# Kernel optimization log

Measured on AMD Instinct MI355X. Metric: run time of the kernel, lower is better.

The kernel has to match this reference:

```python
import jax, jax.numpy as jnp
import numpy as np

N_NODES = 50000
N_EDGES = 800000
DIMS = [64, 128, 128, 64]  # input_dim -> hidden_dims
OUT_DIM = 64
N_CLASSES = 10


def _linear_params(key, in_f, out_f):
    kw, kb = jax.random.split(key)
    bound = 1.0 / np.sqrt(in_f)
    W = jax.random.uniform(kw, (out_f, in_f), jnp.float32, -bound, bound)
    b = jax.random.uniform(kb, (out_f,), jnp.float32, -bound, bound)
    return W, b


def setup_inputs() -> dict:
    key = jax.random.key(0)
    ks = jax.random.split(key, 8)
    x = jax.random.normal(ks[0], (N_NODES, DIMS[0]), jnp.float32)
    edge_index = jax.random.randint(ks[1], (2, N_EDGES), 0, N_NODES, jnp.int32)
    W1, b1 = _linear_params(ks[2], DIMS[0], DIMS[1])
    W2, b2 = _linear_params(ks[3], DIMS[1], DIMS[2])
    W3, b3 = _linear_params(ks[4], DIMS[2], DIMS[3])
    Wp, bp = _linear_params(ks[5], DIMS[3], OUT_DIM)
    Wc, bc = _linear_params(ks[6], DIMS[3], N_CLASSES)
    return {"node_features": x, "edge_index": edge_index,
            "W1": W1, "b1": b1, "W2": W2, "b2": b2, "W3": W3, "b3": b3,
            "Wp": Wp, "bp": bp, "Wc": Wc, "bc": bc}


def _conv_layer(x, src, dst, W, b):
    # mean-aggregate neighbor features via segment_sum over destination nodes
    n = x.shape[0]
    agg = jax.ops.segment_sum(x[src], dst, num_segments=n)  # [N, F]
    deg = jax.ops.segment_sum(jnp.ones_like(dst, jnp.float32), dst, num_segments=n)
    deg = jnp.maximum(deg, 1.0)
    agg = agg / deg[:, None]
    return jax.nn.relu((agg + x) @ W.T + b)


def reference(node_features, edge_index, W1, b1, W2, b2, W3, b3, Wp, bp, Wc, bc):
    src, dst = edge_index[0], edge_index[1]
    x = node_features
    # dropout is identity in eval mode
    x = _conv_layer(x, src, dst, W1, b1)
    x = _conv_layer(x, src, dst, W2, b2)
    x = _conv_layer(x, src, dst, W3, b3)
    node_embeddings = x
    next_event = x @ Wp.T + bp
    event_classes = x @ Wc.T + bc
    return node_embeddings, next_event, event_classes
```

## Files before the change

### kernel.cpp

```cpp
#include <hip/hip_runtime.h>
#include <hip/hip_bf16.h>

typedef __attribute__((ext_vector_type(8))) short short8;
typedef __attribute__((ext_vector_type(4))) float floatx4;

#define NB   196
#define NBLK 256

__device__ __forceinline__ float bf_lo(unsigned int u) { return __uint_as_float(u << 16); }
__device__ __forceinline__ float bf_hi(unsigned int u) { return __uint_as_float(u & 0xffff0000u); }

__device__ __forceinline__ unsigned short f2bf_rne(float f) {
    unsigned u = __float_as_uint(f);
    unsigned rb = (u >> 16) & 1u;
    u += 0x7fffu + rb;
    return (unsigned short)(u >> 16);
}
__device__ __forceinline__ unsigned int pack_bf2(float x, float y) {
    return (unsigned int)f2bf_rne(x) | ((unsigned int)f2bf_rne(y) << 16);
}

__device__ __forceinline__ void acc4(unsigned long long v, float& f0, float& f1, float& f2, float& f3) {
    unsigned ua = (unsigned)v, ub = (unsigned)(v >> 32);
    f0 += bf_lo(ua); f1 += bf_hi(ua); f2 += bf_lo(ub); f3 += bf_hi(ub);
}


__global__ __launch_bounds__(256) void prep_kernel(const int* __restrict__ dst,
                                                   int* __restrict__ blockcnt,
                                                   int E,
                                                   const float* __restrict__ x,
                                                   const float* __restrict__ W1,
                                                   const float* __restrict__ W2,
                                                   const float* __restrict__ W3,
                                                   const float* __restrict__ Wp, const float* __restrict__ bp,
                                                   const float* __restrict__ Wc, const float* __restrict__ bc,
                                                   unsigned int* __restrict__ xb,
                                                   unsigned int* __restrict__ W1b,
                                                   unsigned int* __restrict__ W2b,
                                                   unsigned int* __restrict__ W3b,
                                                   unsigned int* __restrict__ Whb,
                                                   float* __restrict__ hbias,
                                                   int nx) {
    if ((int)blockIdx.x < NBLK) {
        __shared__ int hist[NB];
        for (int i = threadIdx.x; i < NB; i += 256) hist[i] = 0;
        __syncthreads();
        const int chunk = (E + NBLK - 1) / NBLK;
        const int lo = blockIdx.x * chunk;
        const int hi = min(lo + chunk, E);
        for (int e = lo + threadIdx.x; e < hi; e += 256)
            atomicAdd(&hist[dst[e] >> 8], 1);
        __syncthreads();
        for (int i = threadIdx.x; i < NB; i += 256)
            blockcnt[i * NBLK + blockIdx.x] = hist[i];
        return;
    }
    int i = (blockIdx.x - NBLK) * 256 + threadIdx.x;
    const int T0 = nx;
    const int T1 = T0 + 4096;
    const int T2 = T1 + 8192;
    const int T3 = T2 + 4096;
    const int T4 = T3 + 2560;
    const int T5 = T4 + 80;
    if (i < T0) {
        float2 f = ((const float2*)x)[i];
        xb[i] = pack_bf2(f.x, f.y);
    } else if (i < T1) {
        float2 f = ((const float2*)W1)[i - T0];
        W1b[i - T0] = pack_bf2(f.x, f.y);
    } else if (i < T2) {
        float2 f = ((const float2*)W2)[i - T1];
        W2b[i - T1] = pack_bf2(f.x, f.y);
    } else if (i < T3) {
        float2 f = ((const float2*)W3)[i - T2];
        W3b[i - T2] = pack_bf2(f.x, f.y);
    } else if (i < T4) {
        int j = i - T3;
        int r = j >> 5, c = (j & 31) * 2;
        float v0 = 0.f, v1 = 0.f;
        if (r < 64)      { v0 = Wp[r * 64 + c]; v1 = Wp[r * 64 + c + 1]; }
        else if (r < 74) { v0 = Wc[(r - 64) * 64 + c]; v1 = Wc[(r - 64) * 64 + c + 1]; }
        Whb[j] = pack_bf2(v0, v1);
    } else if (i < T5) {
        int j = i - T4;
        float v = 0.f;
        if (j < 64)      v = bp[j];
        else if (j < 74) v = bc[j - 64];
        hbias[j] = v;
    }
}


__global__ __launch_bounds__(256) void partial_sum_kernel(const int* __restrict__ v,
                                                          int* __restrict__ partial, int n) {
    __shared__ int s[256];
    int t = threadIdx.x;
    int i = blockIdx.x * 256 + t;
    s[t] = (i < n) ? v[i] : 0;
    __syncthreads();
    for (int off = 128; off > 0; off >>= 1) {
        if (t < off) s[t] += s[t + off];
        __syncthreads();
    }
    if (t == 0) partial[blockIdx.x] = s[0];
}

__global__ __launch_bounds__(256) void local_scan_kernel(const int* __restrict__ v,
                                                         const int* __restrict__ partial,
                                                         int* __restrict__ base,
                                                         int nblocks, int n) {
    __shared__ int sp[256];
    __shared__ int s[256];
    int t = threadIdx.x;
    sp[t] = (t < nblocks) ? partial[t] : 0;
    __syncthreads();
    for (int off = 1; off < 256; off <<= 1) {
        int u = (t >= off) ? sp[t - off] : 0;
        __syncthreads();
        sp[t] += u;
        __syncthreads();
    }
    const int blockbase = (blockIdx.x == 0) ? 0 : sp[blockIdx.x - 1];
    if (blockIdx.x == 0 && t == 0) base[n] = sp[nblocks - 1];

    int i = blockIdx.x * 256 + t;
    int w = (i < n) ? v[i] : 0;
    s[t] = w;
    __syncthreads();
    for (int off = 1; off < 256; off <<= 1) {
        int u = (t >= off) ? s[t - off] : 0;
        __syncthreads();
        s[t] += u;
        __syncthreads();
    }
    if (i < n) base[i] = blockbase + s[t] - w;
}


__global__ __launch_bounds__(256) void binC_kernel(const int* __restrict__ src,
                                                   const int* __restrict__ dst,
                                                   const int* __restrict__ base,
                                                   unsigned int* __restrict__ pairs, int E) {
    __shared__ int bbase[NB];
    __shared__ int cur[NB];
    for (int i = threadIdx.x; i < NB; i += 256) {
        bbase[i] = base[i * NBLK + blockIdx.x];
        cur[i] = 0;
    }
    __syncthreads();
    const int chunk = (E + NBLK - 1) / NBLK;
    const int lo = blockIdx.x * chunk;
    const int hi = min(lo + chunk, E);
    for (int e = lo + threadIdx.x; e < hi; e += 256) {
        int d = dst[e];
        int b = d >> 8;
        int r = atomicAdd(&cur[b], 1);
        pairs[bbase[b] + r] = ((unsigned)d << 16) | (unsigned)src[e];
    }
}


__global__ __launch_bounds__(256) void bucketD_kernel(const unsigned int* __restrict__ pairs,
                                                      const int* __restrict__ base,
                                                      int* __restrict__ offsets,
                                                      unsigned short* __restrict__ csr_src,
                                                      int E, int n) {
    __shared__ int cnt[256];
    __shared__ int loc[256];
    const int b = blockIdx.x;
    const int start = base[b * NBLK];
    const int end   = base[(b + 1) * NBLK];
    const int t = threadIdx.x;

    cnt[t] = 0;
    __syncthreads();
    for (int i = start + t; i < end; i += 256)
        atomicAdd(&cnt[(pairs[i] >> 16) & 255], 1);
    __syncthreads();

    loc[t] = cnt[t];
    __syncthreads();
    for (int off = 1; off < 256; off <<= 1) {
        int u = (t >= off) ? loc[t - off] : 0;
        __syncthreads();
        loc[t] += u;
        __syncthreads();
    }
    const int excl = (t == 0) ? 0 : loc[t - 1];

    const int d = (b << 8) + t;
    if (d < n) offsets[d] = start + excl;
    if (b == 0 && t == 0) offsets[n] = E;

    __syncthreads();
    cnt[t] = excl;
    __syncthreads();
    for (int i = start + t; i < end; i += 256) {
        unsigned pr = pairs[i];
        int j = (pr >> 16) & 255;
        int p = atomicAdd(&cnt[j], 1);
        csr_src[start + p] = (unsigned short)(pr & 0xffffu);
    }
}


template <int F_IN, int F_OUT, int MODE>
__global__ __launch_bounds__(512) void fused_agg_gemm_kernel(
        const unsigned long long* __restrict__ xt,
        const int* __restrict__ offsets,
        const unsigned short* __restrict__ csr_src,
        const unsigned short* __restrict__ Wb,
        const float* __restrict__ bias,
        unsigned short* __restrict__ Yb,
        float* __restrict__ Yf,
        float* __restrict__ nev, float* __restrict__ cls,
        const unsigned short* __restrict__ Whb, const float* __restrict__ hbias,
        int n) {
    constexpr int KC   = F_IN / 32;
    constexpr int XSTR = F_IN / 4;
    constexpr int HSTR = F_IN + 8;
    __shared__ __align__(16) unsigned short Ht[32 * HSTR];
    __shared__ __align__(16) unsigned short Yt[(MODE == 3) ? 32 * 72 : 16];

    const int lane = threadIdx.x & 63;
    const int wv   = threadIdx.x >> 6;
    const int m0   = blockIdx.x * 32;

    if (F_IN == 64) {
        const int g   = lane >> 4;
        const int c   = lane & 15;
        const int row = wv * 4 + g;
        const int node = m0 + row;
        int ns = 0, ne = 0;
        if (node < n) { ns = offsets[node]; ne = offsets[node + 1]; }
        const int cnt = ne - ns;
        unsigned long long sv = (node < n) ? xt[(size_t)node * XSTR + c] : 0ull;

        int mc = cnt;
        mc = max(mc, __shfl(mc, lane ^ 16, 64));
        mc = max(mc, __shfl(mc, lane ^ 32, 64));

        float s0 = 0.f, s1 = 0.f, s2 = 0.f, s3 = 0.f;
        int ii0 = ns + c;
        if (cnt > 0) { if (ii0 >= ne) ii0 = ne - 1; } else ii0 = 0;
        int idx = (mc > 0) ? (int)csr_src[ii0] : 0;

        for (int base = 0; base < mc; base += 16) {
            int idxN = 0;
            if (base + 16 < mc) {
                int ii = ns + base + 16 + c;
                if (cnt > 0) { if (ii >= ne) ii = ne - 1; } else ii = 0;
                idxN = csr_src[ii];
            }
            unsigned long long v[16];
#pragma unroll
            for (int q = 0; q < 16; ++q) {
                int nb = __shfl(idx, g * 16 + q, 64);
                if (base + q < cnt) v[q] = xt[(size_t)nb * XSTR + c];
            }
#pragma unroll
            for (int q = 0; q < 16; ++q)
                if (base + q < cnt) acc4(v[q], s0, s1, s2, s3);
            idx = idxN;
        }
        float inv = 1.0f / fmaxf((float)cnt, 1.0f);
        unsigned ua = (unsigned)sv, ub = (unsigned)(sv >> 32);
        unsigned o0 = pack_bf2(s0 * inv + bf_lo(ua), s1 * inv + bf_hi(ua));
        unsigned o1 = pack_bf2(s2 * inv + bf_lo(ub), s3 * inv + bf_hi(ub));
        *(unsigned long long*)&Ht[row * HSTR + c * 4] =
            ((unsigned long long)o1 << 32) | o0;
    } else {
        const int g = lane >> 5;
        const int c = lane & 31;
        const int row0 = wv * 4 + g;
        const int row1 = wv * 4 + 2 + g;
        const int node0 = m0 + row0, node1 = m0 + row1;
        int ns0 = 0, ne0 = 0, ns1 = 0, ne1 = 0;
        if (node0 < n) { ns0 = offsets[node0]; ne0 = offsets[node0 + 1]; }
        if (node1 < n) { ns1 = offsets[node1]; ne1 = offsets[node1 + 1]; }
        const int cnt0 = ne0 - ns0, cnt1 = ne1 - ns1;
        unsigned long long sv0 = (node0 < n) ? xt[(size_t)node0 * XSTR + c] : 0ull;
        unsigned long long sv1 = (node1 < n) ? xt[(size_t)node1 * XSTR + c] : 0ull;
        int mc0 = max(cnt0, __shfl(cnt0, lane ^ 32, 64));
        int mc1 = max(cnt1, __shfl(cnt1, lane ^ 32, 64));
        int iiA = ns0 + (c & 15);
        if (cnt0 > 0) { if (iiA >= ne0) iiA = ne0 - 1; } else iiA = 0;
        int iiB = ns1 + (c & 15);
        if (cnt1 > 0) { if (iiB >= ne1) iiB = ne1 - 1; } else iiB = 0;
        int idx0 = (mc0 > 0) ? (int)csr_src[iiA] : 0;
        int idx1 = (mc1 > 0) ? (int)csr_src[iiB] : 0;

        {
            float s0 = 0.f, s1 = 0.f, s2 = 0.f, s3 = 0.f;
            int idx = idx0;
            for (int base = 0; base < mc0; base += 16) {
                int idxN = 0;
                if (base + 16 < mc0) {
                    int ii = ns0 + base + 16 + (c & 15);
                    if (cnt0 > 0) { if (ii >= ne0) ii = ne0 - 1; } else ii = 0;
                    idxN = csr_src[ii];
                }
                unsigned long long v[16];
#pragma unroll
                for (int q = 0; q < 16; ++q) {
                    int nb = __shfl(idx, g * 32 + q, 64);
                    if (base + q < cnt0) v[q] = xt[(size_t)nb * XSTR + c];
                }
#pragma unroll
                for (int q = 0; q < 16; ++q)
                    if (base + q < cnt0) acc4(v[q], s0, s1, s2, s3);
                idx = idxN;
            }
            float inv = 1.0f / fmaxf((float)cnt0, 1.0f);
            unsigned ua = (unsigned)sv0, ub = (unsigned)(sv0 >> 32);
            unsigned o0 = pack_bf2(s0 * inv + bf_lo(ua), s1 * inv + bf_hi(ua));
            unsigned o1 = pack_bf2(s2 * inv + bf_lo(ub), s3 * inv + bf_hi(ub));
            *(unsigned long long*)&Ht[row0 * HSTR + c * 4] =
                ((unsigned long long)o1 << 32) | o0;
        }
        {
            float s0 = 0.f, s1 = 0.f, s2 = 0.f, s3 = 0.f;
            int idx = idx1;
            for (int base = 0; base < mc1; base += 16) {
                int idxN = 0;
                if (base + 16 < mc1) {
                    int ii = ns1 + base + 16 + (c & 15);
                    if (cnt1 > 0) { if (ii >= ne1) ii = ne1 - 1; } else ii = 0;
                    idxN = csr_src[ii];
                }
                unsigned long long v[16];
#pragma unroll
                for (int q = 0; q < 16; ++q) {
                    int nb = __shfl(idx, g * 32 + q, 64);
                    if (base + q < cnt1) v[q] = xt[(size_t)nb * XSTR + c];
                }
#pragma unroll
                for (int q = 0; q < 16; ++q)
                    if (base + q < cnt1) acc4(v[q], s0, s1, s2, s3);
                idx = idxN;
            }
            float inv = 1.0f / fmaxf((float)cnt1, 1.0f);
            unsigned ua = (unsigned)sv1, ub = (unsigned)(sv1 >> 32);
            unsigned o0 = pack_bf2(s0 * inv + bf_lo(ua), s1 * inv + bf_hi(ua));
            unsigned o1 = pack_bf2(s2 * inv + bf_lo(ub), s3 * inv + bf_hi(ub));
            *(unsigned long long*)&Ht[row1 * HSTR + c * 4] =
                ((unsigned long long)o1 << 32) | o0;
        }
    }
    __syncthreads();

    const int quad = lane >> 4;
    const int r16  = lane & 15;

    if (MODE == 0) {
        const int rowg = wv & 1;
        const int cg0  = (wv >> 1) * 2;
        short8 a[KC];
#pragma unroll
        for (int c = 0; c < KC; ++c)
            a[c] = *(const short8*)&Ht[(16 * rowg + r16) * HSTR + 32 * c + quad * 8];

        floatx4 acc[2];
#pragma unroll
        for (int j = 0; j < 2; ++j)
#pragma unroll
            for (int r = 0; r < 4; ++r) acc[j][r] = 0.f;

#pragma unroll
        for (int j = 0; j < 2; ++j)
#pragma unroll
            for (int c = 0; c < KC; ++c) {
                short8 b = *(const short8*)&Wb[(size_t)(16 * (cg0 + j) + r16) * F_IN + 32 * c + quad * 8];
                acc[j] = __builtin_amdgcn_mfma_f32_16x16x32_bf16(a[c], b, acc[j], 0, 0, 0);
            }

#pragma unroll
        for (int r = 0; r < 4; ++r) {
            const int mm = m0 + 16 * rowg + quad * 4 + r;
            if (mm >= n) continue;
#pragma unroll
            for (int j = 0; j < 2; ++j) {
                const int o = 16 * (cg0 + j) + r16;
                Yb[(size_t)mm * F_OUT + o] = f2bf_rne(fmaxf(acc[j][r] + bias[o], 0.f));
            }
        }
    } else {
        const int rowg = wv & 1;
        const int cg   = wv >> 1;
        short8 a[KC];
#pragma unroll
        for (int c = 0; c < KC; ++c)
            a[c] = *(const short8*)&Ht[(16 * rowg + r16) * HSTR + 32 * c + quad * 8];

        floatx4 acc;
#pragma unroll
        for (int r = 0; r < 4; ++r) acc[r] = 0.f;

#pragma unroll
        for (int c = 0; c < KC; ++c) {
            short8 b = *(const short8*)&Wb[(size_t)(16 * cg + r16) * F_IN + 32 * c + quad * 8];
            acc = __builtin_amdgcn_mfma_f32_16x16x32_bf16(a[c], b, acc, 0, 0, 0);
        }

#pragma unroll
        for (int r = 0; r < 4; ++r) {
            const int lr = 16 * rowg + quad * 4 + r;
            const int mm = m0 + lr;
            const int o  = 16 * cg + r16;
            if (mm < n) {
                float v = fmaxf(acc[r] + bias[o], 0.f);
                Yf[(size_t)mm * 64 + o] = v;
                Yt[lr * 72 + o] = f2bf_rne(v);
            } else {
                Yt[lr * 72 + o] = 0;
            }
        }
        __syncthreads();

        for (int t = wv; t < 10; t += 8) {
            const int rg  = t & 1;
            const int cg2 = t >> 1;
            short8 a2[2];
#pragma unroll
            for (int c = 0; c < 2; ++c)
                a2[c] = *(const short8*)&Yt[(16 * rg + r16) * 72 + 32 * c + quad * 8];

            floatx4 acc2;
#pragma unroll
            for (int r = 0; r < 4; ++r) acc2[r] = 0.f;

#pragma unroll
            for (int c = 0; c < 2; ++c) {
                short8 b = *(const short8*)&Whb[(size_t)(16 * cg2 + r16) * 64 + 32 * c + quad * 8];
                acc2 = __builtin_amdgcn_mfma_f32_16x16x32_bf16(a2[c], b, acc2, 0, 0, 0);
            }

#pragma unroll
            for (int r = 0; r < 4; ++r) {
                const int mm = m0 + 16 * rg + quad * 4 + r;
                if (mm >= n) continue;
                const int o = 16 * cg2 + r16;
                float v = acc2[r] + hbias[o];
                if (o < 64)      nev[(size_t)mm * 64 + o] = v;
                else if (o < 74) cls[(size_t)mm * 10 + (o - 64)] = v;
            }
        }
    }
}


extern "C" void kernel_launch(void* const* d_in, const int* in_sizes, int n_in,
                              void* d_out, int out_size, void* d_ws, size_t ws_size,
                              hipStream_t stream) {
    const float* x  = (const float*)d_in[0];
    const int*   ei = (const int*)d_in[1];
    const float* W1 = (const float*)d_in[2];
    const float* b1 = (const float*)d_in[3];
    const float* W2 = (const float*)d_in[4];
    const float* b2 = (const float*)d_in[5];
    const float* W3 = (const float*)d_in[6];
    const float* b3 = (const float*)d_in[7];
    const float* Wp = (const float*)d_in[8];
    const float* bp = (const float*)d_in[9];
    const float* Wc = (const float*)d_in[10];
    const float* bc = (const float*)d_in[11];

    const int n = in_sizes[0] / 64;
    const int E = in_sizes[1] / 2;
    const int* src = ei;
    const int* dst = ei + E;

    const int items = NB * NBLK;
    const int nScan = (items + 255) / 256;

    int* blockcnt = (int*)d_ws;
    int* base     = blockcnt + items;
    int* partial  = base + items + 1;
    int* offsets  = partial + 256;
    unsigned int*   pairs   = (unsigned int*)(offsets + n + 1);
    unsigned short* csr_src = (unsigned short*)(pairs + E);
    uintptr_t p = (uintptr_t)(csr_src + E);
    p = (p + 255) & ~(uintptr_t)255;
    unsigned int* Hb  = (unsigned int*)p;
    unsigned int* Yb  = Hb + (size_t)n * 64;
    unsigned int* xb  = Yb + (size_t)n * 64;
    unsigned int* W1b = xb + (size_t)n * 32;
    unsigned int* W2b = W1b + 4096;
    unsigned int* W3b = W2b + 8192;
    unsigned int* Whb = W3b + 4096;
    float* hbias = (float*)(Whb + 2560);

    float* out_emb = (float*)d_out;
    float* out_nev = out_emb + (size_t)n * 64;
    float* out_cls = out_nev + (size_t)n * 64;

    const int convTotal = n * 32 + 4096 + 8192 + 4096 + 2560 + 80;
    const int convBlocks = (convTotal + 255) / 256;
    prep_kernel<<<NBLK + convBlocks, 256, 0, stream>>>(
        dst, blockcnt, E,
        x, W1, W2, W3, Wp, bp, Wc, bc, xb, W1b, W2b, W3b, Whb, hbias, n * 32);

    partial_sum_kernel<<<nScan, 256, 0, stream>>>(blockcnt, partial, items);
    local_scan_kernel<<<nScan, 256, 0, stream>>>(blockcnt, partial, base, nScan, items);

    binC_kernel<<<NBLK, 256, 0, stream>>>(src, dst, base, pairs, E);
    bucketD_kernel<<<NB, 256, 0, stream>>>(pairs, base, offsets, csr_src, E, n);

    const int gF = (n + 31) / 32;

    fused_agg_gemm_kernel<64, 128, 0><<<gF, 512, 0, stream>>>(
        (const unsigned long long*)xb, offsets, csr_src,
        (const unsigned short*)W1b, b1, (unsigned short*)Hb,
        nullptr, nullptr, nullptr, nullptr, nullptr, n);

    fused_agg_gemm_kernel<128, 128, 0><<<gF, 512, 0, stream>>>(
        (const unsigned long long*)Hb, offsets, csr_src,
        (const unsigned short*)W2b, b2, (unsigned short*)Yb,
        nullptr, nullptr, nullptr, nullptr, nullptr, n);

    fused_agg_gemm_kernel<128, 64, 3><<<gF, 512, 0, stream>>>(
        (const unsigned long long*)Yb, offsets, csr_src,
        (const unsigned short*)W3b, b3, nullptr,
        out_emb, out_nev, out_cls, (const unsigned short*)Whb, hbias, n);
}
```

Measured before the change: 230.2 us.

## Split fused aggregate+GEMM into column-sliced gather kernels and separate MFMA GEMMs

Replaces each fused aggregate-then-GEMM kernel with two kernels. The first aggregates neighbours per node over a column slice of 8 uint64 lanes, spreading the edges across 8 lane groups and combining them with a shuffle reduction. The second runs a standalone MFMA GEMM that reads the aggregated bf16 rows from a workspace buffer. Slicing columns is meant to keep each slice's gather working set in cache and balance work across skewed degrees. The cost is three extra launches and an extra write and read of the aggregated matrix through global memory.

```diff
diff --git a/kernel.cpp b/kernel.cpp
--- a/kernel.cpp
+++ b/kernel.cpp
@@ -205,243 +205,164 @@
 }
 
 
-template <int F_IN, int F_OUT, int MODE>
-__global__ __launch_bounds__(512) void fused_agg_gemm_kernel(
+template <int F_IN, int NSLICE>
+__global__ __launch_bounds__(256) void agg_slice_kernel(
         const unsigned long long* __restrict__ xt,
         const int* __restrict__ offsets,
         const unsigned short* __restrict__ csr_src,
-        const unsigned short* __restrict__ Wb,
-        const float* __restrict__ bias,
-        unsigned short* __restrict__ Yb,
-        float* __restrict__ Yf,
-        float* __restrict__ nev, float* __restrict__ cls,
-        const unsigned short* __restrict__ Whb, const float* __restrict__ hbias,
+        unsigned long long* __restrict__ hb,
         int n) {
-    constexpr int KC   = F_IN / 32;
     constexpr int XSTR = F_IN / 4;
-    constexpr int HSTR = F_IN + 8;
-    __shared__ __align__(16) unsigned short Ht[32 * HSTR];
-    __shared__ __align__(16) unsigned short Yt[(MODE == 3) ? 32 * 72 : 16];
-
     const int lane = threadIdx.x & 63;
     const int wv   = threadIdx.x >> 6;
-    const int m0   = blockIdx.x * 32;
-
-    if (F_IN == 64) {
-        const int g   = lane >> 4;
-        const int c   = lane & 15;
-        const int row = wv * 4 + g;
-        const int node = m0 + row;
-        int ns = 0, ne = 0;
-        if (node < n) { ns = offsets[node]; ne = offsets[node + 1]; }
+    const int s    = blockIdx.x % NSLICE;
+    const int nb   = blockIdx.x / NSLICE;
+    const int g    = lane >> 3;
+    const int c    = lane & 7;
+    const int col  = s * 8 + c;
+
+#pragma unroll 1
+    for (int i = 0; i < 4; ++i) {
+        const int node = nb * 16 + wv * 4 + i;
+        if (node >= n) continue;
+        const int ns = offsets[node];
+        const int ne = offsets[node + 1];
         const int cnt = ne - ns;
-        unsigned long long sv = (node < n) ? xt[(size_t)node * XSTR + c] : 0ull;
-
-        int mc = cnt;
-        mc = max(mc, __shfl(mc, lane ^ 16, 64));
-        mc = max(mc, __shfl(mc, lane ^ 32, 64));
+        unsigned long long sv = xt[(size_t)node * XSTR + col];
 
         float s0 = 0.f, s1 = 0.f, s2 = 0.f, s3 = 0.f;
-        int ii0 = ns + c;
-        if (cnt > 0) { if (ii0 >= ne) ii0 = ne - 1; } else ii0 = 0;
-        int idx = (mc > 0) ? (int)csr_src[ii0] : 0;
-
-        for (int base = 0; base < mc; base += 16) {
-            int idxN = 0;
-            if (base + 16 < mc) {
-                int ii = ns + base + 16 + c;
-                if (cnt > 0) { if (ii >= ne) ii = ne - 1; } else ii = 0;
-                idxN = csr_src[ii];
+        for (int base = 0; base < cnt; base += 64) {
+            int ii = ns + base + lane; if (ii >= ne) ii = ne - 1;
+            int idx = csr_src[ii];
+            int m = cnt - base; if (m > 64) m = 64;
+            unsigned long long v[8];
+#pragma unroll
+            for (int q = 0; q < 8; ++q) {
+                int nb2 = __shfl(idx, q * 8 + g, 64);
+                if (q * 8 + g < m) v[q] = xt[(size_t)nb2 * XSTR + col];
             }
-            unsigned long long v[16];
-#pragma unroll
-            for (int q = 0; q < 16; ++q) {
-                int nb = __shfl(idx, g * 16 + q, 64);
-                if (base + q < cnt) v[q] = xt[(size_t)nb * XSTR + c];
-            }
-#pragma unroll
-            for (int q = 0; q < 16; ++q)
-                if (base + q < cnt) acc4(v[q], s0, s1, s2, s3);
-            idx = idxN;
+#pragma unroll
+            for (int q = 0; q < 8; ++q)
+                if (q * 8 + g < m) acc4(v[q], s0, s1, s2, s3);
         }
-        float inv = 1.0f / fmaxf((float)cnt, 1.0f);
-        unsigned ua = (unsigned)sv, ub = (unsigned)(sv >> 32);
-        unsigned o0 = pack_bf2(s0 * inv + bf_lo(ua), s1 * inv + bf_hi(ua));
-        unsigned o1 = pack_bf2(s2 * inv + bf_lo(ub), s3 * inv + bf_hi(ub));
-        *(unsigned long long*)&Ht[row * HSTR + c * 4] =
-            ((unsigned long long)o1 << 32) | o0;
-    } else {
-        const int g = lane >> 5;
-        const int c = lane & 31;
-        const int row0 = wv * 4 + g;
-        const int row1 = wv * 4 + 2 + g;
-        const int node0 = m0 + row0, node1 = m0 + row1;
-        int ns0 = 0, ne0 = 0, ns1 = 0, ne1 = 0;
-        if (node0 < n) { ns0 = offsets[node0]; ne0 = offsets[node0 + 1]; }
-        if (node1 < n) { ns1 = offsets[node1]; ne1 = offsets[node1 + 1]; }
-        const int cnt0 = ne0 - ns0, cnt1 = ne1 - ns1;
-        unsigned long long sv0 = (node0 < n) ? xt[(size_t)node0 * XSTR + c] : 0ull;
-        unsigned long long sv1 = (node1 < n) ? xt[(size_t)node1 * XSTR + c] : 0ull;
-        int mc0 = max(cnt0, __shfl(cnt0, lane ^ 32, 64));
-        int mc1 = max(cnt1, __shfl(cnt1, lane ^ 32, 64));
-        int iiA = ns0 + (c & 15);
-        if (cnt0 > 0) { if (iiA >= ne0) iiA = ne0 - 1; } else iiA = 0;
-        int iiB = ns1 + (c & 15);
-        if (cnt1 > 0) { if (iiB >= ne1) iiB = ne1 - 1; } else iiB = 0;
-        int idx0 = (mc0 > 0) ? (int)csr_src[iiA] : 0;
-        int idx1 = (mc1 > 0) ? (int)csr_src[iiB] : 0;
-
-        {
-            float s0 = 0.f, s1 = 0.f, s2 = 0.f, s3 = 0.f;
-            int idx = idx0;
-            for (int base = 0; base < mc0; base += 16) {
-                int idxN = 0;
-                if (base + 16 < mc0) {
-                    int ii = ns0 + base + 16 + (c & 15);
-                    if (cnt0 > 0) { if (ii >= ne0) ii = ne0 - 1; } else ii = 0;
-                    idxN = csr_src[ii];
-                }
-                unsigned long long v[16];
-#pragma unroll
-                for (int q = 0; q < 16; ++q) {
-                    int nb = __shfl(idx, g * 32 + q, 64);
-                    if (base + q < cnt0) v[q] = xt[(size_t)nb * XSTR + c];
-                }
-#pragma unroll
-                for (int q = 0; q < 16; ++q)
-                    if (base + q < cnt0) acc4(v[q], s0, s1, s2, s3);
-                idx = idxN;
-            }
-            float inv = 1.0f / fmaxf((float)cnt0, 1.0f);
-            unsigned ua = (unsigned)sv0, ub = (unsigned)(sv0 >> 32);
+        s0 += __shfl(s0, lane ^ 8, 64);  s1 += __shfl(s1, lane ^ 8, 64);
+        s2 += __shfl(s2, lane ^ 8, 64);  s3 += __shfl(s3, lane ^ 8, 64);
+        s0 += __shfl(s0, lane ^ 16, 64); s1 += __shfl(s1, lane ^ 16, 64);
+        s2 += __shfl(s2, lane ^ 16, 64); s3 += __shfl(s3, lane ^ 16, 64);
+        s0 += __shfl(s0, lane ^ 32, 64); s1 += __shfl(s1, lane ^ 32, 64);
+        s2 += __shfl(s2, lane ^ 32, 64); s3 += __shfl(s3, lane ^ 32, 64);
+
+        if (g == 0) {
+            float inv = 1.0f / fmaxf((float)cnt, 1.0f);
+            unsigned ua = (unsigned)sv, ub = (unsigned)(sv >> 32);
             unsigned o0 = pack_bf2(s0 * inv + bf_lo(ua), s1 * inv + bf_hi(ua));
             unsigned o1 = pack_bf2(s2 * inv + bf_lo(ub), s3 * inv + bf_hi(ub));
-            *(unsigned long long*)&Ht[row0 * HSTR + c * 4] =
-                ((unsigned long long)o1 << 32) | o0;
+            hb[(size_t)node * XSTR + col] = ((unsigned long long)o1 << 32) | o0;
         }
-        {
-            float s0 = 0.f, s1 = 0.f, s2 = 0.f, s3 = 0.f;
-            int idx = idx1;
-            for (int base = 0; base < mc1; base += 16) {
-                int idxN = 0;
-                if (base + 16 < mc1) {
-                    int ii = ns1 + base + 16 + (c & 15);
-                    if (cnt1 > 0) { if (ii >= ne1) ii = ne1 - 1; } else ii = 0;
-                    idxN = csr_src[ii];
-                }
-                unsigned long long v[16];
-#pragma unroll
-                for (int q = 0; q < 16; ++q) {
-                    int nb = __shfl(idx, g * 32 + q, 64);
-                    if (base + q < cnt1) v[q] = xt[(size_t)nb * XSTR + c];
-                }
-#pragma unroll
-                for (int q = 0; q < 16; ++q)
-                    if (base + q < cnt1) acc4(v[q], s0, s1, s2, s3);
-                idx = idxN;
-            }
-            float inv = 1.0f / fmaxf((float)cnt1, 1.0f);
-            unsigned ua = (unsigned)sv1, ub = (unsigned)(sv1 >> 32);
-            unsigned o0 = pack_bf2(s0 * inv + bf_lo(ua), s1 * inv + bf_hi(ua));
-            unsigned o1 = pack_bf2(s2 * inv + bf_lo(ub), s3 * inv + bf_hi(ub));
-            *(unsigned long long*)&Ht[row1 * HSTR + c * 4] =
-                ((unsigned long long)o1 << 32) | o0;
-        }
-    }
-    __syncthreads();
-
+    }
+}
+
+
+template <int F_IN, int F_OUT, int MODE>
+__global__ __launch_bounds__(256) void mfma_gemm_kernel(const unsigned short* __restrict__ Hb,
+                                                        const unsigned short* __restrict__ Wb,
+                                                        const float* __restrict__ bias,
+                                                        unsigned short* __restrict__ Yb,
+                                                        float* __restrict__ Yf,
+                                                        float* __restrict__ nev,
+                                                        float* __restrict__ cls,
+                                                        const unsigned short* __restrict__ Whb,
+                                                        const float* __restrict__ hbias,
+                                                        int n) {
+    constexpr int KC = F_IN / 32;
+    constexpr int NJ = F_OUT / 16;
+    __shared__ unsigned short Ytile[(MODE == 3) ? 64 * 72 : 1];
+
+    const int lane = threadIdx.x & 63;
+    const int wv   = threadIdx.x >> 6;
     const int quad = lane >> 4;
     const int r16  = lane & 15;
-
-    if (MODE == 0) {
-        const int rowg = wv & 1;
-        const int cg0  = (wv >> 1) * 2;
-        short8 a[KC];
+    const int m0   = blockIdx.x * 64 + wv * 16;
+
+    short8 a[KC];
+    const int am = m0 + r16;
+    if (am < n) {
 #pragma unroll
         for (int c = 0; c < KC; ++c)
-            a[c] = *(const short8*)&Ht[(16 * rowg + r16) * HSTR + 32 * c + quad * 8];
-
-        floatx4 acc[2];
-#pragma unroll
-        for (int j = 0; j < 2; ++j)
-#pragma unroll
-            for (int r = 0; r < 4; ++r) acc[j][r] = 0.f;
-
-#pragma unroll
-        for (int j = 0; j < 2; ++j)
-#pragma unroll
-            for (int c = 0; c < KC; ++c) {
-                short8 b = *(const short8*)&Wb[(size_t)(16 * (cg0 + j) + r16) * F_IN + 32 * c + quad * 8];
-                acc[j] = __builtin_amdgcn_mfma_f32_16x16x32_bf16(a[c], b, acc[j], 0, 0, 0);
-            }
-
-#pragma unroll
-        for (int r = 0; r < 4; ++r) {
-            const int mm = m0 + 16 * rowg + quad * 4 + r;
-            if (mm >= n) continue;
-#pragma unroll
-            for (int j = 0; j < 2; ++j) {
-                const int o = 16 * (cg0 + j) + r16;
-                Yb[(size_t)mm * F_OUT + o] = f2bf_rne(fmaxf(acc[j][r] + bias[o], 0.f));
+            a[c] = *(const short8*)&Hb[(size_t)am * F_IN + 32 * c + quad * 8];
+    } else {
+#pragma unroll
+        for (int c = 0; c < KC; ++c)
+#pragma unroll
+            for (int i = 0; i < 8; ++i) a[c][i] = 0;
+    }
+
+    floatx4 acc[NJ];
+#pragma unroll
+    for (int j = 0; j < NJ; ++j)
+#pragma unroll
+        for (int r = 0; r < 4; ++r) acc[j][r] = 0.f;
+
+#pragma unroll
+    for (int j = 0; j < NJ; ++j) {
+#pragma unroll
+        for (int c = 0; c < KC; ++c) {
+            short8 b = *(const short8*)&Wb[(size_t)(16 * j + r16) * F_IN + 32 * c + quad * 8];
+            acc[j] = __builtin_amdgcn_mfma_f32_16x16x32_bf16(a[c], b, acc[j], 0, 0, 0);
+        }
+    }
+
+#pragma unroll
+    for (int r = 0; r < 4; ++r) {
+        const int mm = m0 + quad * 4 + r;
+        const int lrow = wv * 16 + quad * 4 + r;
+#pragma unroll
+        for (int j = 0; j < NJ; ++j) {
+            const int o = 16 * j + r16;
+            if (mm < n) {
+                float v = fmaxf(acc[j][r] + bias[o], 0.f);
+                if (MODE == 0) {
+                    Yb[(size_t)mm * F_OUT + o] = f2bf_rne(v);
+                } else {
+                    Yf[(size_t)mm * 64 + o] = v;
+                    Ytile[lrow * 72 + o] = f2bf_rne(v);
+                }
+            } else if (MODE == 3) {
+                Ytile[lrow * 72 + o] = 0;
             }
         }
-    } else {
-        const int rowg = wv & 1;
-        const int cg   = wv >> 1;
-        short8 a[KC];
-#pragma unroll
-        for (int c = 0; c < KC; ++c)
-            a[c] = *(const short8*)&Ht[(16 * rowg + r16) * HSTR + 32 * c + quad * 8];
-
-        floatx4 acc;
-#pragma unroll
-        for (int r = 0; r < 4; ++r) acc[r] = 0.f;
-
-#pragma unroll
-        for (int c = 0; c < KC; ++c) {
-            short8 b = *(const short8*)&Wb[(size_t)(16 * cg + r16) * F_IN + 32 * c + quad * 8];
-            acc = __builtin_amdgcn_mfma_f32_16x16x32_bf16(a[c], b, acc, 0, 0, 0);
-        }
+    }
+
+    if (MODE == 3) {
+        __syncthreads();
+
+        short8 a2[2];
+#pragma unroll
+        for (int c = 0; c < 2; ++c)
+            a2[c] = *(const short8*)&Ytile[(wv * 16 + r16) * 72 + 32 * c + quad * 8];
+
+        floatx4 acc2[5];
+#pragma unroll
+        for (int j = 0; j < 5; ++j)
+#pragma unroll
+            for (int r = 0; r < 4; ++r) acc2[j][r] = 0.f;
+
+#pragma unroll
+        for (int j = 0; j < 5; ++j)
+#pragma unroll
+            for (int c = 0; c < 2; ++c) {
+                short8 b = *(const short8*)&Whb[(size_t)(16 * j + r16) * 64 + 32 * c + quad * 8];
+                acc2[j] = __builtin_amdgcn_mfma_f32_16x16x32_bf16(a2[c], b, acc2[j], 0, 0, 0);
+            }
 
 #pragma unroll
         for (int r = 0; r < 4; ++r) {
-            const int lr = 16 * rowg + quad * 4 + r;
-            const int mm = m0 + lr;
-            const int o  = 16 * cg + r16;
-            if (mm < n) {
-                float v = fmaxf(acc[r] + bias[o], 0.f);
-                Yf[(size_t)mm * 64 + o] = v;
-                Yt[lr * 72 + o] = f2bf_rne(v);
-            } else {
-                Yt[lr * 72 + o] = 0;
-            }
-        }
-        __syncthreads();
-
-        for (int t = wv; t < 10; t += 8) {
-            const int rg  = t & 1;
-            const int cg2 = t >> 1;
-            short8 a2[2];
-#pragma unroll
-            for (int c = 0; c < 2; ++c)
-                a2[c] = *(const short8*)&Yt[(16 * rg + r16) * 72 + 32 * c + quad * 8];
-
-            floatx4 acc2;
-#pragma unroll
-            for (int r = 0; r < 4; ++r) acc2[r] = 0.f;
-
-#pragma unroll
-            for (int c = 0; c < 2; ++c) {
-                short8 b = *(const short8*)&Whb[(size_t)(16 * cg2 + r16) * 64 + 32 * c + quad * 8];
-                acc2 = __builtin_amdgcn_mfma_f32_16x16x32_bf16(a2[c], b, acc2, 0, 0, 0);
-            }
-
-#pragma unroll
-            for (int r = 0; r < 4; ++r) {
-                const int mm = m0 + 16 * rg + quad * 4 + r;
-                if (mm >= n) continue;
-                const int o = 16 * cg2 + r16;
-                float v = acc2[r] + hbias[o];
+            const int mm = m0 + quad * 4 + r;
+            if (mm >= n) continue;
+#pragma unroll
+            for (int j = 0; j < 5; ++j) {
+                const int o = 16 * j + r16;
+                float v = acc2[j][r] + hbias[o];
                 if (o < 64)      nev[(size_t)mm * 64 + o] = v;
                 else if (o < 74) cls[(size_t)mm * 10 + (o - 64)] = v;
             }
@@ -482,7 +403,8 @@
     unsigned short* csr_src = (unsigned short*)(pairs + E);
     uintptr_t p = (uintptr_t)(csr_src + E);
     p = (p + 255) & ~(uintptr_t)255;
-    unsigned int* Hb  = (unsigned int*)p;
+    unsigned int* Ab  = (unsigned int*)p;
+    unsigned int* Hb  = Ab + (size_t)n * 64;
     unsigned int* Yb  = Hb + (size_t)n * 64;
     unsigned int* xb  = Yb + (size_t)n * 64;
     unsigned int* W1b = xb + (size_t)n * 32;
@@ -507,20 +429,24 @@
     binC_kernel<<<NBLK, 256, 0, stream>>>(src, dst, base, pairs, E);
     bucketD_kernel<<<NB, 256, 0, stream>>>(pairs, base, offsets, csr_src, E, n);
 
-    const int gF = (n + 31) / 32;
-
-    fused_agg_gemm_kernel<64, 128, 0><<<gF, 512, 0, stream>>>(
-        (const unsigned long long*)xb, offsets, csr_src,
-        (const unsigned short*)W1b, b1, (unsigned short*)Hb,
-        nullptr, nullptr, nullptr, nullptr, nullptr, n);
-
-    fused_agg_gemm_kernel<128, 128, 0><<<gF, 512, 0, stream>>>(
-        (const unsigned long long*)Hb, offsets, csr_src,
-        (const unsigned short*)W2b, b2, (unsigned short*)Yb,
-        nullptr, nullptr, nullptr, nullptr, nullptr, n);
-
-    fused_agg_gemm_kernel<128, 64, 3><<<gF, 512, 0, stream>>>(
-        (const unsigned long long*)Yb, offsets, csr_src,
-        (const unsigned short*)W3b, b3, nullptr,
-        out_emb, out_nev, out_cls, (const unsigned short*)Whb, hbias, n);
-}
+    const int nNB = (n + 15) / 16;
+    const int gMf = (n + 63) / 64;
+
+    agg_slice_kernel<64, 2><<<nNB * 2, 256, 0, stream>>>(
+        (const unsigned long long*)xb, offsets, csr_src, (unsigned long long*)Ab, n);
+    mfma_gemm_kernel<64, 128, 0><<<gMf, 256, 0, stream>>>(
+        (const unsigned short*)Ab, (const unsigned short*)W1b, b1,
+        (unsigned short*)Hb, nullptr, nullptr, nullptr, nullptr, nullptr, n);
+
+    agg_slice_kernel<128, 4><<<nNB * 4, 256, 0, stream>>>(
+        (const unsigned long long*)Hb, offsets, csr_src, (unsigned long long*)Ab, n);
+    mfma_gemm_kernel<128, 128, 0><<<gMf, 256, 0, stream>>>(
+        (const unsigned short*)Ab, (const unsigned short*)W2b, b2,
+        (unsigned short*)Yb, nullptr, nullptr, nullptr, nullptr, nullptr, n);
+
+    agg_slice_kernel<128, 4><<<nNB * 4, 256, 0, stream>>>(
+        (const unsigned long long*)Yb, offsets, csr_src, (unsigned long long*)Ab, n);
+    mfma_gemm_kernel<128, 64, 3><<<gMf, 256, 0, stream>>>(
+        (const unsigned short*)Ab, (const unsigned short*)W3b, b3,
+        nullptr, out_emb, out_nev, out_cls, (const unsigned short*)Whb, hbias, n);
+}
```

New measurement: 348.7 us. 51.5% more time.
